# Performance work log

Hardware: AMD Instinct MI355X
Metric: run time of the kernel (lower is better)

## Reference

```python
import jax, jax.numpy as jnp
import numpy as np

B, S, D, H = 4, 2048, 1024, 16
HD = D // H  # head_dim = 64


def setup_inputs() -> dict:
    key = jax.random.key(0)
    ks = jax.random.split(key, 5)
    s = 1.0 / np.sqrt(D)
    return {
        "x": jax.random.normal(ks[0], (B, S, D), jnp.float32),
        "Wq": jax.random.normal(ks[1], (D, D), jnp.float32) * s,
        "Wk": jax.random.normal(ks[2], (D, D), jnp.float32) * s,
        "Wv": jax.random.normal(ks[3], (D, D), jnp.float32) * s,
        "Wo": jax.random.normal(ks[4], (D, D), jnp.float32) * s,
        "bo": jnp.zeros((D,), jnp.float32),
    }


def reference(x, Wq, Wk, Wv, Wo, bo):
    b, s, d = x.shape
    # projections (torch Linear: x @ W.T; weights here stored as [in, out] equivalent)
    q = (x @ Wq).reshape(b, s, H, HD).transpose(0, 2, 1, 3)  # [b,h,s,hd]
    k = (x @ Wk).reshape(b, s, H, HD).transpose(0, 2, 1, 3)
    v = (x @ Wv).reshape(b, s, H, HD).transpose(0, 2, 1, 3)
    scores = jnp.einsum("bhqd,bhkd->bhqk", q, k) * (HD ** -0.5)
    causal = jnp.tril(jnp.ones((s, s), bool))  # mask==0 -> -inf
    scores = jnp.where(causal, scores, -jnp.inf)
    attn = jax.nn.softmax(scores, axis=-1)
    out = jnp.einsum("bhqk,bhkd->bhqd", attn, v)
    out = out.transpose(0, 2, 1, 3).reshape(b, s, d)
    return out @ Wo + bo
```

## Files before the change

kernel.cpp:

```cpp
#include <hip/hip_runtime.h>
#include <cstdint>
#include <cstddef>

typedef __attribute__((ext_vector_type(8))) short bf16x8;
typedef __attribute__((ext_vector_type(4))) short bf16x4;
typedef __attribute__((ext_vector_type(4))) float f32x4;

constexpr int Bsz = 4, Ssz = 2048, Dsz = 1024, Hn = 16, HDsz = 64;
constexpr int Msz = Bsz * Ssz;
constexpr float LOG2E = 1.4426950408889634f;

#define MFMA16(a, b, c) __builtin_amdgcn_mfma_f32_16x16x16bf16_1k(a, b, c, 0, 0, 0)

__device__ __forceinline__ unsigned short f2bf(float f) {
  union { float f; unsigned int u; } v; v.f = f;
  unsigned int r = v.u + 0x7fffu + ((v.u >> 16) & 1u);
  return (unsigned short)(r >> 16);
}

typedef __attribute__((address_space(1))) const unsigned int gu32;
typedef __attribute__((address_space(3))) unsigned int lu32;
__device__ __forceinline__ void async_cp16(const unsigned short* g, unsigned short* l) {
  __builtin_amdgcn_global_load_lds((gu32*)g, (lu32*)l, 16, 0, 0);
}

__global__ void prep_kernel(const float* __restrict__ x, unsigned short* __restrict__ xb,
                            const float* __restrict__ W0, const float* __restrict__ W1,
                            const float* __restrict__ W2, const float* __restrict__ W3,
                            unsigned short* __restrict__ T0, unsigned short* __restrict__ T1,
                            unsigned short* __restrict__ T2, unsigned short* __restrict__ T3) {
  const int z = blockIdx.z;
  if (z == 4) {
    const int i0 = (blockIdx.y * 32 + blockIdx.x) * 2048 + threadIdx.x;
#pragma unroll
    for (int j = 0; j < 8; j++) {
      const int i = i0 + j * 256;
      const float4 v = reinterpret_cast<const float4*>(x)[i];
      ushort4 o;
      o.x = f2bf(v.x); o.y = f2bf(v.y); o.z = f2bf(v.z); o.w = f2bf(v.w);
      reinterpret_cast<ushort4*>(xb)[i] = o;
    }
    return;
  }
  __shared__ float tile[32][33];
  const float* W = (z == 0) ? W0 : (z == 1) ? W1 : (z == 2) ? W2 : W3;
  unsigned short* Wt = (z == 0) ? T0 : (z == 1) ? T1 : (z == 2) ? T2 : T3;
  int tx = threadIdx.x & 31, ty = threadIdx.x >> 5;
  int bx = blockIdx.x, by = blockIdx.y;
#pragma unroll
  for (int i = 0; i < 4; i++) {
    int k = by * 32 + ty + i * 8;
    tile[ty + i * 8][tx] = W[k * Dsz + bx * 32 + tx];
  }
  __syncthreads();
#pragma unroll
  for (int i = 0; i < 4; i++) {
    int nrow = bx * 32 + ty + i * 8;
    Wt[nrow * Dsz + by * 32 + tx] = f2bf(tile[tx][ty + i * 8]);
  }
}

enum { EPI_QKV = 0, EPI_OUT = 1 };

template <int EPI>
__global__ __launch_bounds__(512, 4)
void gemm_bk64(const unsigned short* __restrict__ A,
               const unsigned short* __restrict__ Bt,
               unsigned short* __restrict__ Qh,
               unsigned short* __restrict__ Kh,
               unsigned short* __restrict__ Vth,
               float* __restrict__ Out,
               const float* __restrict__ bias) {
  __shared__ unsigned short As[128 * 64];
  __shared__ unsigned short Bs[128 * 64];

  const int tid = threadIdx.x;
  const int w = tid >> 6, lane = tid & 63;
  const int l15 = lane & 15, quad = lane >> 4;
  const int wr = w >> 1, wc = w & 1;
  const int bm = blockIdx.y, bn = blockIdx.x;
  const int rr = lane >> 3;
  const int scoff = ((lane & 7) ^ rr) * 8;

  f32x4 acc[2][4];
#pragma unroll
  for (int i = 0; i < 2; i++)
#pragma unroll
    for (int j = 0; j < 4; j++) acc[i][j] = (f32x4){0.f, 0.f, 0.f, 0.f};

  const int rowA0 = bm * 128, rowB0 = bn * 128;

  for (int kt = 0; kt < Dsz / 64; kt++) {
#pragma unroll
    for (int i = 0; i < 2; i++) {
      const int r8 = w * 16 + i * 8;
      async_cp16(&A[(size_t)(rowA0 + r8 + rr) * Dsz + kt * 64 + scoff], &As[r8 * 64]);
      async_cp16(&Bt[(size_t)(rowB0 + r8 + rr) * Dsz + kt * 64 + scoff], &Bs[r8 * 64]);
    }
    __syncthreads();

#pragma unroll
    for (int ks = 0; ks < 2; ks++) {
      bf16x8 af[2], bfr[4];
#pragma unroll
      for (int t = 0; t < 2; t++) {
        const int ra = wr * 32 + t * 16 + l15;
        af[t] = *reinterpret_cast<const bf16x8*>(
            &As[ra * 64 + (((ks * 4 + quad) ^ (ra & 7)) * 8)]);
      }
#pragma unroll
      for (int t = 0; t < 4; t++) {
        const int rb = wc * 64 + t * 16 + l15;
        bfr[t] = *reinterpret_cast<const bf16x8*>(
            &Bs[rb * 64 + (((ks * 4 + quad) ^ (rb & 7)) * 8)]);
      }
#pragma unroll
      for (int i = 0; i < 2; i++)
#pragma unroll
        for (int j = 0; j < 4; j++)
          acc[i][j] = __builtin_amdgcn_mfma_f32_16x16x32_bf16(af[i], bfr[j], acc[i][j], 0, 0, 0);
    }
    __syncthreads();
  }

  if (EPI == EPI_QKV) {
    const int proj = (bn * 128) >> 10;
#pragma unroll
    for (int i = 0; i < 2; i++) {
#pragma unroll
      for (int j = 0; j < 4; j++) {
        const int n = bn * 128 + wc * 64 + j * 16 + l15;
        const int nn = n & 1023, h = nn >> 6, hd = nn & 63;
        const int m0 = bm * 128 + wr * 32 + i * 16 + quad * 4;
        const int b = m0 >> 11, s0 = m0 & (Ssz - 1);
        if (proj == 0) {
#pragma unroll
          for (int r = 0; r < 4; r++)
            Qh[((size_t)(b * Hn + h) * Ssz + s0 + r) * HDsz + hd] =
                f2bf(acc[i][j][r] * (0.125f * LOG2E));
        } else if (proj == 1) {
#pragma unroll
          for (int r = 0; r < 4; r++)
            Kh[((size_t)(b * Hn + h) * Ssz + s0 + r) * HDsz + hd] = f2bf(acc[i][j][r]);
        } else {
          ushort4 o;
          o.x = f2bf(acc[i][j][0]); o.y = f2bf(acc[i][j][1]);
          o.z = f2bf(acc[i][j][2]); o.w = f2bf(acc[i][j][3]);
          *reinterpret_cast<ushort4*>(
              &Vth[((size_t)(b * Hn + h) * HDsz + hd) * Ssz + s0]) = o;
        }
      }
    }
  } else {
#pragma unroll
    for (int i = 0; i < 2; i++) {
#pragma unroll
      for (int j = 0; j < 4; j++) {
        const int n = bn * 128 + wc * 64 + j * 16 + l15;
        const int m0 = bm * 128 + wr * 32 + i * 16 + quad * 4;
#pragma unroll
        for (int r = 0; r < 4; r++)
          Out[(size_t)(m0 + r) * Dsz + n] = acc[i][j][r] + bias[n];
      }
    }
  }
}

__global__ __launch_bounds__(256, 4)
void flash_kernel(const unsigned short* __restrict__ Q,
                  const unsigned short* __restrict__ Kg,
                  const unsigned short* __restrict__ Vt,
                  unsigned short* __restrict__ AO) {
  __shared__ unsigned short Ks[64 * 64];
  __shared__ unsigned short Vs[64 * 64];

  const int tid = threadIdx.x;
  const int w = tid >> 6, lane = tid & 63;
  const int l15 = lane & 15, quad = lane >> 4;
  const int rr = lane >> 3;

  const int linear = blockIdx.y * 16 + blockIdx.x;
  const int bh = (linear & 7) * 8 + ((linear >> 3) & 7);
  const int g = linear >> 6, gk = g >> 2, ga = g & 3;
  const int t = (gk == 0) ? 15 - ga : (gk == 1) ? 8 + ga : (gk == 2) ? 7 - ga : ga;

  const unsigned short* Qb = Q + (size_t)bh * Ssz * HDsz;
  const unsigned short* Kb = Kg + (size_t)bh * Ssz * HDsz;
  const unsigned short* Vb = Vt + (size_t)bh * HDsz * Ssz;
  const int b = bh / Hn, h = bh % Hn;

  const int hl = (l15 & 7) ^ ((l15 >> 3) << 2);

  const int q0 = t * 128;
  const int rowStart = q0 + w * 32;

  bf16x8 qf[2][2];
#pragma unroll
  for (int tm = 0; tm < 2; tm++)
#pragma unroll
    for (int ks = 0; ks < 2; ks++)
      qf[tm][ks] = *reinterpret_cast<const bf16x8*>(
          &Qb[(size_t)(rowStart + tm * 16 + l15) * HDsz + ks * 32 + quad * 8]);

  f32x4 oacc[2][4];
  float lpart[2] = {0.f, 0.f};
#pragma unroll
  for (int tm = 0; tm < 2; tm++)
#pragma unroll
    for (int tn = 0; tn < 4; tn++) oacc[tm][tn] = (f32x4){0.f, 0.f, 0.f, 0.f};

  const int nkb = 2 * t + 2;
  for (int kb = 0; kb < nkb; kb++) {
    const int kv0 = kb * 64;
#pragma unroll
    for (int i = 0; i < 2; i++) {
      const int r8 = w * 16 + i * 8;
      const int sc = (((lane & 7) ^ rr ^ (i << 2))) * 8;
      async_cp16(&Kb[(size_t)(kv0 + r8 + rr) * HDsz + sc], &Ks[r8 * 64]);
      async_cp16(&Vb[(size_t)(r8 + rr) * Ssz + kv0 + sc], &Vs[r8 * 64]);
    }
    __syncthreads();

    const bool skip = (kv0 >= rowStart + 32);
    if (!skip) {
      f32x4 sc[4][2];
#pragma unroll
      for (int tn = 0; tn < 4; tn++)
#pragma unroll
        for (int tm = 0; tm < 2; tm++) sc[tn][tm] = (f32x4){0.f, 0.f, 0.f, 0.f};
#pragma unroll
      for (int ks = 0; ks < 2; ks++) {
#pragma unroll
        for (int tn = 0; tn < 4; tn++) {
          const int rk = tn * 16 + l15;
          bf16x8 kf = *reinterpret_cast<const bf16x8*>(
              &Ks[rk * 64 + (((ks * 4 + quad) ^ hl) * 8)]);
#pragma unroll
          for (int tm = 0; tm < 2; tm++)
            sc[tn][tm] = __builtin_amdgcn_mfma_f32_16x16x32_bf16(kf, qf[tm][ks], sc[tn][tm], 0, 0, 0);
        }
      }

      const bool needMask = (kv0 + 63 > rowStart);
      if (needMask) {
#pragma unroll
        for (int tn = 0; tn < 4; tn++)
#pragma unroll
          for (int tm = 0; tm < 2; tm++) {
            const int qrow = rowStart + tm * 16 + l15;
#pragma unroll
            for (int r = 0; r < 4; r++)
              if (kv0 + tn * 16 + quad * 4 + r > qrow) sc[tn][tm][r] = -1e30f;
          }
      }

      unsigned int pk[4][2][2];
#pragma unroll
      for (int tn = 0; tn < 4; tn++)
#pragma unroll
        for (int tm = 0; tm < 2; tm++) {
          union { float f; unsigned int u; } e0, e1, e2, e3;
          e0.f = __builtin_amdgcn_exp2f(sc[tn][tm][0]);
          e1.f = __builtin_amdgcn_exp2f(sc[tn][tm][1]);
          e2.f = __builtin_amdgcn_exp2f(sc[tn][tm][2]);
          e3.f = __builtin_amdgcn_exp2f(sc[tn][tm][3]);
          lpart[tm] += (e0.f + e1.f) + (e2.f + e3.f);
          pk[tn][tm][0] = __builtin_amdgcn_perm(e1.u, e0.u, 0x07060302u);
          pk[tn][tm][1] = __builtin_amdgcn_perm(e3.u, e2.u, 0x07060302u);
        }

#pragma unroll
      for (int tn = 0; tn < 4; tn++) {
        bf16x4 pa[2];
#pragma unroll
        for (int tm = 0; tm < 2; tm++) {
          union { unsigned int u[2]; bf16x4 v; } cv;
          cv.u[0] = pk[tn][tm][0]; cv.u[1] = pk[tn][tm][1];
          pa[tm] = cv.v;
        }
#pragma unroll
        for (int to = 0; to < 4; to++) {
          const int rv = to * 16 + l15;
          const int chunk = tn * 2 + (quad >> 1);
          bf16x4 vf = *reinterpret_cast<const bf16x4*>(
              (const char*)Vs + rv * 128 + ((chunk ^ hl) * 16) + (quad & 1) * 8);
#pragma unroll
          for (int tm = 0; tm < 2; tm++)
            oacc[tm][to] = MFMA16(pa[tm], vf, oacc[tm][to]);
        }
      }
    }
    __syncthreads();
  }

#pragma unroll
  for (int tm = 0; tm < 2; tm++) {
    float lf = lpart[tm];
    lf += __shfl_xor(lf, 16);
    lf += __shfl_xor(lf, 32);
    float linv[4];
#pragma unroll
    for (int r = 0; r < 4; r++) {
      union { float f; int i; } cv;
      cv.f = lf;
      cv.i = __builtin_amdgcn_ds_bpermute((quad * 4 + r) * 4, cv.i);
      linv[r] = 1.f / cv.f;
    }
#pragma unroll
    for (int r = 0; r < 4; r++) {
      const int s = rowStart + tm * 16 + quad * 4 + r;
      const size_t m = (size_t)b * Ssz + s;
#pragma unroll
      for (int tn = 0; tn < 4; tn++) {
        const int n = h * HDsz + tn * 16 + l15;
        AO[m * Dsz + n] = f2bf(oacc[tm][tn][r] * linv[r]);
      }
    }
  }
}

extern "C" void kernel_launch(void* const* d_in, const int* in_sizes, int n_in,
                              void* d_out, int out_size, void* d_ws, size_t ws_size,
                              hipStream_t stream) {
  const float* x  = (const float*)d_in[0];
  const float* Wq = (const float*)d_in[1];
  const float* Wk = (const float*)d_in[2];
  const float* Wv = (const float*)d_in[3];
  const float* Wo = (const float*)d_in[4];
  const float* bo = (const float*)d_in[5];
  float* out = (float*)d_out;

  unsigned short* xb  = (unsigned short*)d_ws;
  unsigned short* Wqt = xb + (size_t)Msz * Dsz;
  unsigned short* Wkt = Wqt + (size_t)Dsz * Dsz;
  unsigned short* Wvt = Wkt + (size_t)Dsz * Dsz;
  unsigned short* Wot = Wvt + (size_t)Dsz * Dsz;
  unsigned short* Qh  = Wot + (size_t)Dsz * Dsz;
  unsigned short* Kh  = Qh + (size_t)Msz * Dsz;
  unsigned short* Vth = Kh + (size_t)Msz * Dsz;
  unsigned short* AO  = Vth + (size_t)Msz * Dsz;

  prep_kernel<<<dim3(32, 32, 5), 256, 0, stream>>>(
      x, xb, Wq, Wk, Wv, Wo, Wqt, Wkt, Wvt, Wot);

  gemm_bk64<EPI_QKV><<<dim3(3 * Dsz / 128, Msz / 128), 512, 0, stream>>>(
      xb, Wqt, Qh, Kh, Vth, nullptr, nullptr);

  flash_kernel<<<dim3(16, Bsz * Hn), 256, 0, stream>>>(Qh, Kh, Vth, AO);

  gemm_bk64<EPI_OUT><<<dim3(Dsz / 128, Msz / 128), 512, 0, stream>>>(
      AO, Wot, nullptr, nullptr, nullptr, out, bo);
}
```

Baseline: 233.0 us.

## Replace QKV projection GEMM with 256x256 tiled, phase-pipelined async-copy kernel

Adds a dedicated QKV projection GEMM that uses 256x256 output tiles with double-buffered LDS fed by global_load_lds. The K loop is split into four phases with explicit barriers, vmcnt waits and raised priority around the MFMA blocks, so copies for the next tile overlap with compute. A swizzled block order is meant to improve L2 reuse. This should cut global traffic per FLOP and hide load latency, at the cost of much more LDS (128KB per block), a high register count and fragile hand-placed waitcnt logic.

```diff
diff --git a/kernel.cpp b/kernel.cpp
--- a/kernel.cpp
+++ b/kernel.cpp
@@ -5,12 +5,14 @@
 typedef __attribute__((ext_vector_type(8))) short bf16x8;
 typedef __attribute__((ext_vector_type(4))) short bf16x4;
 typedef __attribute__((ext_vector_type(4))) float f32x4;
+typedef unsigned short us;
 
 constexpr int Bsz = 4, Ssz = 2048, Dsz = 1024, Hn = 16, HDsz = 64;
 constexpr int Msz = Bsz * Ssz;
 constexpr float LOG2E = 1.4426950408889634f;
 
 #define MFMA16(a, b, c) __builtin_amdgcn_mfma_f32_16x16x16bf16_1k(a, b, c, 0, 0, 0)
+#define MFMA32(a, b, c) __builtin_amdgcn_mfma_f32_16x16x32_bf16(a, b, c, 0, 0, 0)
 
 __device__ __forceinline__ unsigned short f2bf(float f) {
   union { float f; unsigned int u; } v; v.f = f;
@@ -118,7 +120,7 @@
       for (int i = 0; i < 2; i++)
 #pragma unroll
         for (int j = 0; j < 4; j++)
-          acc[i][j] = __builtin_amdgcn_mfma_f32_16x16x32_bf16(af[i], bfr[j], acc[i][j], 0, 0, 0);
+          acc[i][j] = MFMA32(af[i], bfr[j], acc[i][j]);
     }
     __syncthreads();
   }
@@ -166,6 +168,156 @@
   }
 }
 
+#define BARRIER() do { asm volatile("" ::: "memory"); __builtin_amdgcn_s_barrier(); asm volatile("" ::: "memory"); } while (0)
+#define LGKM0() asm volatile("s_waitcnt lgkmcnt(0)" ::: "memory")
+#define VMW6()  asm volatile("s_waitcnt vmcnt(6)" ::: "memory")
+#define VMW0()  asm volatile("s_waitcnt vmcnt(0)" ::: "memory")
+#define CFENCE() asm volatile("" ::: "memory")
+
+#define PHASE_TAIL(P, AF)                                                   \
+  BARRIER(); LGKM0();                                                       \
+  __builtin_amdgcn_s_setprio(1);                                            \
+  _Pragma("unroll")                                                         \
+  for (int ks = 0; ks < 2; ks++)                                            \
+    _Pragma("unroll")                                                       \
+    for (int im = 0; im < 2; im++)                                          \
+      _Pragma("unroll")                                                     \
+      for (int n = 0; n < 4; n++)                                           \
+        acc[2 * (P) + im][n] = MFMA32(AF[im][ks], bfr[n][ks], acc[2 * (P) + im][n]); \
+  __builtin_amdgcn_s_setprio(0);
+
+#define KTILE(Ac, Bc, Ao, Bo, U) do {                                       \
+  const int u_ = (U);                                                       \
+  {   \
+    bf16x8 af[2][2];                                                        \
+    rdB(Bc);                                                                \
+    rdA(Ac, 0, af);                                                         \
+    if (u_ + 1 < 16) { stA(Ao, 3, u_ + 1); stB(Bo, 3, u_ + 1); }            \
+    PHASE_TAIL(0, af); BARRIER();                                           \
+  }                                                                         \
+  {                                                            \
+    bf16x8 af[2][2];                                                        \
+    rdA(Ac, 1, af);                                                         \
+    if (u_ + 2 < 16) { stA(Ac, 0, u_ + 2); stB(Bc, 0, u_ + 2); }            \
+    PHASE_TAIL(1, af); BARRIER();                                           \
+  }                                                                         \
+  {                                                            \
+    bf16x8 af[2][2];                                                        \
+    rdA(Ac, 2, af);                                                         \
+    if (u_ + 2 < 16) { stA(Ac, 1, u_ + 2); stB(Bc, 1, u_ + 2); }            \
+    PHASE_TAIL(2, af); BARRIER();                                           \
+  }                                                                         \
+  {                    \
+    bf16x8 af[2][2];                                                        \
+    rdA(Ac, 3, af);                                                         \
+    if (u_ + 2 < 16) { stA(Ac, 2, u_ + 2); stB(Bc, 2, u_ + 2); }            \
+    PHASE_TAIL(3, af);                                                      \
+    if (u_ < 14) { VMW6(); } else if (u_ == 14) { VMW0(); }                 \
+    BARRIER();                                                              \
+  }                                                                         \
+} while (0)
+
+__global__ __launch_bounds__(512, 2)
+void gemm256_qkv(const us* __restrict__ A, const us* __restrict__ Bt,
+                 us* __restrict__ Qh, us* __restrict__ Kh, us* __restrict__ Vth) {
+  __shared__ us As0[256 * 64];
+  __shared__ us Bs0[256 * 64];
+  __shared__ us As1[256 * 64];
+  __shared__ us Bs1[256 * 64];
+
+  const int tid = threadIdx.x;
+  const int w = tid >> 6, lane = tid & 63;
+  const int l15 = lane & 15, quad = lane >> 4;
+  const int wr = w >> 2, wc = w & 3;
+  const int rr = lane >> 3;
+  const int sc16 = ((lane & 7) ^ rr) * 8;
+
+  const int orig = blockIdx.y * 12 + blockIdx.x;
+  const int swz = (orig & 7) * 48 + (orig >> 3);
+  const int bn = swz / 32, bm = swz % 32;
+
+  const size_t rowA0 = (size_t)bm * 256, rowB0 = (size_t)bn * 256;
+
+  f32x4 acc[8][4];
+#pragma unroll
+  for (int i = 0; i < 8; i++)
+#pragma unroll
+    for (int j = 0; j < 4; j++) acc[i][j] = (f32x4){0.f, 0.f, 0.f, 0.f};
+
+  bf16x8 bfr[4][2];
+
+  auto stA = [&](us* L, int stripe, int t) {
+    async_cp16(&A[(rowA0 + stripe * 64 + 8 * w + rr) * (size_t)Dsz + t * 64 + sc16],
+               &L[(stripe * 64 + 8 * w) * 64]);
+  };
+  auto stB = [&](us* L, int stripe, int t) {
+    async_cp16(&Bt[(rowB0 + stripe * 64 + 8 * w + rr) * (size_t)Dsz + t * 64 + sc16],
+               &L[(stripe * 64 + 8 * w) * 64]);
+  };
+  auto rdA = [&](const us* L, int P, bf16x8 (&af)[2][2]) {
+#pragma unroll
+    for (int im = 0; im < 2; im++)
+#pragma unroll
+      for (int ks = 0; ks < 2; ks++) {
+        const int ra = P * 64 + im * 32 + wr * 16 + l15;
+        af[im][ks] = *reinterpret_cast<const bf16x8*>(
+            &L[ra * 64 + (((ks * 4 + quad) ^ (ra & 7)) * 8)]);
+      }
+  };
+  auto rdB = [&](const us* L) {
+#pragma unroll
+    for (int n = 0; n < 4; n++)
+#pragma unroll
+      for (int ks = 0; ks < 2; ks++) {
+        const int rb = wc * 64 + n * 16 + l15;
+        bfr[n][ks] = *reinterpret_cast<const bf16x8*>(
+            &L[rb * 64 + (((ks * 4 + quad) ^ (rb & 7)) * 8)]);
+      }
+  };
+
+#pragma unroll
+  for (int s = 0; s < 4; s++) { stA(As0, s, 0); stB(Bs0, s, 0); }
+  CFENCE();
+#pragma unroll
+  for (int s = 0; s < 3; s++) { stA(As1, s, 1); stB(Bs1, s, 1); }
+  VMW6();
+  BARRIER();
+
+#pragma unroll 1
+  for (int t2 = 0; t2 < 16; t2 += 2) {
+    KTILE(As0, Bs0, As1, Bs1, t2);
+    KTILE(As1, Bs1, As0, Bs0, t2 + 1);
+  }
+
+  const int proj = bn >> 2;
+#pragma unroll
+  for (int i = 0; i < 8; i++) {
+#pragma unroll
+    for (int j = 0; j < 4; j++) {
+      const int n = bn * 256 + wc * 64 + j * 16 + l15;
+      const int nn = n & 1023, h = nn >> 6, hd = nn & 63;
+      const int m0 = bm * 256 + i * 32 + wr * 16 + quad * 4;
+      const int b = m0 >> 11, s0 = m0 & (Ssz - 1);
+      if (proj == 0) {
+#pragma unroll
+        for (int r = 0; r < 4; r++)
+          Qh[((size_t)(b * Hn + h) * Ssz + s0 + r) * HDsz + hd] =
+              f2bf(acc[i][j][r] * (0.125f * LOG2E));
+      } else if (proj == 1) {
+#pragma unroll
+        for (int r = 0; r < 4; r++)
+          Kh[((size_t)(b * Hn + h) * Ssz + s0 + r) * HDsz + hd] = f2bf(acc[i][j][r]);
+      } else {
+        ushort4 o;
+        o.x = f2bf(acc[i][j][0]); o.y = f2bf(acc[i][j][1]);
+        o.z = f2bf(acc[i][j][2]); o.w = f2bf(acc[i][j][3]);
+        *reinterpret_cast<ushort4*>(
+            &Vth[((size_t)(b * Hn + h) * HDsz + hd) * Ssz + s0]) = o;
+      }
+    }
+  }
+}
+
 __global__ __launch_bounds__(256, 4)
 void flash_kernel(const unsigned short* __restrict__ Q,
                   const unsigned short* __restrict__ Kg,
@@ -237,7 +389,7 @@
               &Ks[rk * 64 + (((ks * 4 + quad) ^ hl) * 8)]);
 #pragma unroll
           for (int tm = 0; tm < 2; tm++)
-            sc[tn][tm] = __builtin_amdgcn_mfma_f32_16x16x32_bf16(kf, qf[tm][ks], sc[tn][tm], 0, 0, 0);
+            sc[tn][tm] = MFMA32(kf, qf[tm][ks], sc[tn][tm]);
         }
       }
 
@@ -343,8 +495,7 @@
   prep_kernel<<<dim3(32, 32, 5), 256, 0, stream>>>(
       x, xb, Wq, Wk, Wv, Wo, Wqt, Wkt, Wvt, Wot);
 
-  gemm_bk64<EPI_QKV><<<dim3(3 * Dsz / 128, Msz / 128), 512, 0, stream>>>(
-      xb, Wqt, Qh, Kh, Vth, nullptr, nullptr);
+  gemm256_qkv<<<dim3(12, 32), 512, 0, stream>>>(xb, Wqt, Qh, Kh, Vth);
 
   flash_kernel<<<dim3(16, Bsz * Hn), 256, 0, stream>>>(Qh, Kh, Vth, AO);
 
```

Result: slower. 249.8 us (+7.2%).
